# Kernel optimization log

Measured on AMD Instinct MI355X. Metric: run time of the kernel, lower is better.

The kernel has to match this reference:

```python
import jax, jax.numpy as jnp
import numpy as np
import math

B, S, T, D, H = 4, 1024, 1024, 512, 8
EPS = 1e-5

def setup_inputs() -> dict:
    key = jax.random.key(0)
    ks = iter(jax.random.split(key, 40))
    w = lambda *shp: jax.random.normal(next(ks), shp, jnp.float32) * 0.02
    inp = {
        'x': jax.random.normal(next(ks), (B, S, D), jnp.float32),
        'encod_out': jax.random.normal(next(ks), (B, T, D), jnp.float32),
    }
    for p in ('sa', 'ca'):
        inp[p + '_wq'] = w(H, D, D); inp[p + '_bq'] = w(H, D)
        inp[p + '_wk'] = w(H, D, D); inp[p + '_bk'] = w(H, D)
        inp[p + '_wv'] = w(H, D, D); inp[p + '_bv'] = w(H, D)
        inp[p + '_wo'] = w(H, D, D); inp[p + '_bo'] = w(H, D)
        inp[p + '_wf'] = w(H * D, D); inp[p + '_bf'] = w(D)
    for i in (1, 2, 3):
        inp[f'ln{i}_g'] = jnp.ones((D,), jnp.float32)
        inp[f'ln{i}_b'] = jnp.zeros((D,), jnp.float32)
    inp['fc1_w'] = w(D, 4 * D); inp['fc1_b'] = w(4 * D)
    inp['fc2_w'] = w(4 * D, D); inp['fc2_b'] = w(D)
    return inp

def _ln(x, g, b):
    m = jnp.mean(x, -1, keepdims=True)
    v = jnp.mean((x - m) ** 2, -1, keepdims=True)
    return (x - m) / jnp.sqrt(v + EPS) * g + b

def _mha(xq, xkv, wq, bq, wk, bk, wv, bv, wo, bo, wf, bf, mask):
    # per-head FULL-width projections, stacked on head axis h
    Q = jnp.einsum('bsd,hdf->bhsf', xq, wq) + bq[None, :, None, :]
    K = jnp.einsum('btd,hdf->bhtf', xkv, wk) + bk[None, :, None, :]
    V = jnp.einsum('btd,hdf->bhtf', xkv, wv) + bv[None, :, None, :]
    scores = jnp.einsum('bhsf,bhtf->bhst', Q, K) / math.sqrt(Q.shape[-1])
    if mask is not None:
        scores = jnp.where(mask == 0, -jnp.inf, scores)
    A = jax.nn.softmax(scores, axis=-1)
    O = jnp.einsum('bhst,bhtf->bhsf', A, V)
    O = jnp.einsum('bhsf,hfg->bhsg', O, wo) + bo[None, :, None, :]  # per-head out_linear
    cat = O.transpose(0, 2, 1, 3).reshape(O.shape[0], O.shape[2], -1)  # [B,S,H*D]
    return cat @ wf + bf

def reference(x, encod_out,
              sa_wq, sa_bq, sa_wk, sa_bk, sa_wv, sa_bv, sa_wo, sa_bo, sa_wf, sa_bf,
              ca_wq, ca_bq, ca_wk, ca_bk, ca_wv, ca_bv, ca_wo, ca_bo, ca_wf, ca_bf,
              ln1_g, ln1_b, ln2_g, ln2_b, ln3_g, ln3_b,
              fc1_w, fc1_b, fc2_w, fc2_b):
    s = x.shape[1]
    mask = jnp.tril(jnp.ones((s, s), x.dtype))
    h = _mha(x, x, sa_wq, sa_bq, sa_wk, sa_bk, sa_wv, sa_bv, sa_wo, sa_bo, sa_wf, sa_bf, mask)
    x1 = _ln(h + x, ln1_g, ln1_b)
    h = _mha(x1, encod_out, ca_wq, ca_bq, ca_wk, ca_bk, ca_wv, ca_bv, ca_wo, ca_bo, ca_wf, ca_bf, None)
    x2 = _ln(h + x1, ln2_g, ln2_b)
    ff = jax.nn.relu(x2 @ fc1_w + fc1_b) @ fc2_w + fc2_b
    return _ln(ff + x2, ln3_g, ln3_b)
```

## Files before the change

### kernel.cpp

```cpp
#include <hip/hip_runtime.h>
#include <hip/hip_bf16.h>

typedef __hip_bfloat16 bf16;
typedef __attribute__((ext_vector_type(8))) __bf16 bf16x8;
typedef __attribute__((ext_vector_type(4))) float f32x4;

typedef const __attribute__((address_space(1))) void cg_void;
typedef __attribute__((address_space(3))) void lds_void;

__device__ inline float b2f(bf16 v) { return __bfloat162float(v); }
__device__ inline bf16 f2b(float v) { return __float2bfloat16(v); }
__device__ inline float ldf(const float* p) { return *p; }
__device__ inline float ldf(const bf16* p) { return __bfloat162float(*p); }

#define BKK 32

template<int N> __device__ __forceinline__ void wait_vm() {
  if constexpr (N == 0) asm volatile("s_waitcnt vmcnt(0)" ::: "memory");
  else if constexpr (N == 3) asm volatile("s_waitcnt vmcnt(3)" ::: "memory");
  else if constexpr (N == 6) asm volatile("s_waitcnt vmcnt(6)" ::: "memory");
  else asm volatile("s_waitcnt vmcnt(4)" ::: "memory");
}

template<int BM_, int BN_, bool BIAS, bool RELU, bool OUT_BF16>
__global__ __launch_bounds__(256, 2) void gemm_bt(
    const bf16* __restrict__ A, const bf16* __restrict__ Bt, void* __restrict__ Cout,
    const float* __restrict__ bias,
    int M, int N, int K, int lda, int ldb, int ldc,
    long aHi, long aLo, long bHi, long bLo, long cHi, long cLo, int zdiv, int cmode)
{
  constexpr int MI = BM_ / 32;
  constexpr int NJ = BN_ / 32;
  constexpr int NLA = BM_ / 64;
  constexpr int NLB = BN_ / 64;
  constexpr int NL = NLA + NLB;
  alignas(16) __shared__ bf16 As[3][BM_ * BKK];
  alignas(16) __shared__ bf16 Bs[3][BN_ * BKK];
  const int t = threadIdx.x;
  const int l = t & 63;
  const int w = t >> 6;

  const int gx = gridDim.x;
  const long gxy = (long)gx * gridDim.y;
  long flat = (long)blockIdx.z * gxy + (long)blockIdx.y * gx + blockIdx.x;
  const long total = gxy * gridDim.z;
  if ((total & 7) == 0) flat = (flat & 7) * (total >> 3) + (flat >> 3);
  const int z = (int)(flat / gxy);
  const int rem = (int)(flat % gxy);
  const int m0 = (rem % gx) * BM_;
  const int n0 = (rem / gx) * BN_;

  if (cmode == 1 && n0 >= m0 + BM_) return;

  const int zq = z / zdiv, zr = z % zdiv;
  A += (long)zq * aHi + (long)zr * aLo;
  Bt += (long)zq * bHi + (long)zr * bLo;
  const long cbase = (long)zq * cHi + (long)zr * cLo;

  f32x4 acc[MI][NJ] = {};

  const int r0 = t >> 2;
  const int kcs = ((t & 3) ^ ((t >> 3) & 3)) * 8;
  const bf16* aP0 = A + (long)(m0 + r0) * lda + kcs;
  const bf16* bP0 = Bt + (long)(n0 + r0) * ldb + kcs;

  const int fr = l & 15;
  const int qa = (fr >> 1) & 3;
  const int fko = ((l >> 4) ^ qa) << 3;
  const int aRow = (w >> 1) * (BM_ / 2) + fr;
  const int bRow = (w & 1) * (BN_ / 2) + fr;

  const int kLim = (cmode == 2) ? (m0 + BM_ < K ? m0 + BM_ : K) : K;
  const int nt = kLim >> 5;

  auto stage = [&](int tt, int bi) {
    const long kt = (long)tt * BKK;
#pragma unroll
    for (int u = 0; u < NLA; ++u)
      __builtin_amdgcn_global_load_lds((cg_void*)(aP0 + (long)u * 64 * lda + kt),
                                       (lds_void*)(&As[bi][(t + u * 256) * 8]), 16, 0, 0);
#pragma unroll
    for (int u = 0; u < NLB; ++u)
      __builtin_amdgcn_global_load_lds((cg_void*)(bP0 + (long)u * 64 * ldb + kt),
                                       (lds_void*)(&Bs[bi][(t + u * 256) * 8]), 16, 0, 0);
  };

  stage(0, 0);
  stage(1, 1);
  wait_vm<NL>();
  __builtin_amdgcn_s_barrier();

  int bi = 0;
  for (int tt = 0; tt < nt; ++tt) {
    if (tt + 2 < nt) stage(tt + 2, bi == 0 ? 2 : bi - 1);
    bf16x8 af[MI], bv[NJ];
#pragma unroll
    for (int i = 0; i < MI; ++i)
      af[i] = *(const bf16x8*)(&As[bi][(aRow + i * 16) * BKK + fko]);
#pragma unroll
    for (int j = 0; j < NJ; ++j)
      bv[j] = *(const bf16x8*)(&Bs[bi][(bRow + j * 16) * BKK + fko]);
#pragma unroll
    for (int i = 0; i < MI; ++i)
#pragma unroll
      for (int j = 0; j < NJ; ++j)
        acc[i][j] = __builtin_amdgcn_mfma_f32_16x16x32_bf16(af[i], bv[j], acc[i][j], 0, 0, 0);
    if (tt + 1 < nt) {
      if (tt + 2 < nt) wait_vm<NL>();
      else wait_vm<0>();
      __builtin_amdgcn_s_barrier();
    }
    bi = (bi == 2) ? 0 : bi + 1;
  }

  float* cf = (float*)Cout;
  bf16* cb = (bf16*)Cout;
#pragma unroll
  for (int i = 0; i < MI; ++i) {
    const int mb = m0 + (w >> 1) * (BM_ / 2) + i * 16 + ((l >> 4) << 2);
#pragma unroll
    for (int j = 0; j < NJ; ++j) {
      const int nc = n0 + (w & 1) * (BN_ / 2) + j * 16 + fr;
      const float bvv = BIAS ? bias[nc] : 0.f;
#pragma unroll
      for (int r = 0; r < 4; ++r) {
        const int m = mb + r;
        const long off = cbase + (long)m * ldc + nc;
        float vv = acc[i][j][r] + bvv;
        if (RELU) vv = fmaxf(vv, 0.f);
        if (OUT_BF16) cb[off] = f2b(vv);
        else cf[off] = vv;
      }
    }
  }
}

template<int BM_, int BN_, bool B_, bool R_, bool O_>
static inline void gemmL(hipStream_t st, int M, int N, int K,
                         const bf16* A, int lda, long aHi, long aLo,
                         const bf16* Bt, int ldb, long bHi, long bLo,
                         void* C, int ldc, long cHi, long cLo,
                         int zdiv, int nz, const float* bias, int cmode = 0)
{
  dim3 g(M / BM_, N / BN_, nz);
  gemm_bt<BM_, BN_, B_, R_, O_><<<g, dim3(256), 0, st>>>(
      A, Bt, C, bias, M, N, K, lda, ldb, ldc, aHi, aLo, bHi, bLo, cHi, cLo, zdiv, cmode);
}

template<typename ST>
__global__ __launch_bounds__(256) void transpose_to_bf16(
    const ST* __restrict__ in, bf16* __restrict__ out, int R, int C, long sIn, long sOut)
{
  __shared__ bf16 tile[32][33];
  const int z = blockIdx.z;
  in += (long)z * sIn;
  out += (long)z * sOut;
  const int tx = threadIdx.x & 31, ty = threadIdx.x >> 5;
  const int c0 = blockIdx.x * 32, r0 = blockIdx.y * 32;
#pragma unroll
  for (int i = 0; i < 4; ++i)
    tile[ty + i * 8][tx] = f2b(ldf(in + (long)(r0 + ty + i * 8) * C + c0 + tx));
  __syncthreads();
#pragma unroll
  for (int i = 0; i < 4; ++i)
    out[(long)(c0 + ty + i * 8) * R + r0 + tx] = tile[tx][ty + i * 8];
}

__global__ __launch_bounds__(256) void cast4_k(
    const float* __restrict__ in, bf16* __restrict__ out, long n4)
{
  long i = (long)blockIdx.x * 256 + threadIdx.x;
  const long st = (long)gridDim.x * 256;
  for (; i < n4; i += st) {
    const float4 v = ((const float4*)in)[i];
    bf16* o = out + i * 4;
    o[0] = f2b(v.x); o[1] = f2b(v.y); o[2] = f2b(v.z); o[3] = f2b(v.w);
  }
}

__global__ __launch_bounds__(256) void cast4x4_k(
    const float* __restrict__ p0, const float* __restrict__ p1,
    const float* __restrict__ p2, const float* __restrict__ p3,
    bf16* __restrict__ o0, bf16* __restrict__ o1,
    bf16* __restrict__ o2, bf16* __restrict__ o3, long n4)
{
  const float* in; bf16* out;
  switch (blockIdx.y) {
    case 0: in = p0; out = o0; break;
    case 1: in = p1; out = o1; break;
    case 2: in = p2; out = o2; break;
    default: in = p3; out = o3; break;
  }
  long i = (long)blockIdx.x * 256 + threadIdx.x;
  const long st = (long)gridDim.x * 256;
  for (; i < n4; i += st) {
    const float4 v = ((const float4*)in)[i];
    bf16* o = out + i * 4;
    o[0] = f2b(v.x); o[1] = f2b(v.y); o[2] = f2b(v.z); o[3] = f2b(v.w);
  }
}

__global__ __launch_bounds__(256) void fill_sentinel(float* __restrict__ out, long n)
{
  long i = (long)blockIdx.x * 256 + threadIdx.x;
  const long st = (long)gridDim.x * 256;
  for (; i < n; i += st) out[i] = 1.0e6f;
}

__global__ __launch_bounds__(256) void softmax_rows(
    bf16* __restrict__ S, const float* __restrict__ v, float scale, int causal)
{
  const int r = blockIdx.x * 4 + (threadIdx.x >> 6);
  const int l = threadIdx.x & 63;
  const int zl = r >> 10, s = r & 1023;
  bf16* row = S + (long)r * 1024;
  const float* vp = v + (zl >> 2) * 4096 + (zl & 3) * 1024;
  const int t0 = l * 16;
  bf16x8* rp = (bf16x8*)(row + t0);
  const bf16x8 a0 = rp[0], a1 = rp[1];
  float xx[16];
#pragma unroll
  for (int j = 0; j < 8; ++j) { xx[j] = (float)a0[j]; xx[8 + j] = (float)a1[j]; }
  float mx = -3.4e38f;
#pragma unroll
  for (int k = 0; k < 16; ++k) {
    const int tt = t0 + k;
    float val = (xx[k] + vp[tt]) * scale;
    if (causal && tt > s) val = -3.4e38f;
    xx[k] = val;
    mx = fmaxf(mx, val);
  }
#pragma unroll
  for (int d = 1; d < 64; d <<= 1) mx = fmaxf(mx, __shfl_xor(mx, d));
  float sum = 0.f;
#pragma unroll
  for (int k = 0; k < 16; ++k) {
    const float e = (xx[k] > -1e37f) ? __expf(xx[k] - mx) : 0.f;
    xx[k] = e;
    sum += e;
  }
#pragma unroll
  for (int d = 1; d < 64; d <<= 1) sum += __shfl_xor(sum, d);
  const float inv = 1.f / sum;
  bf16x8 r0v, r1v;
#pragma unroll
  for (int j = 0; j < 8; ++j) {
    r0v[j] = (__bf16)(xx[j] * inv);
    r1v[j] = (__bf16)(xx[8 + j] * inv);
  }
  rp[0] = r0v;
  rp[1] = r1v;
}

__global__ __launch_bounds__(256) void ln_fused(
    const float* __restrict__ parts, long zstride, int nz,
    const float* __restrict__ beff, const float* __restrict__ resF,
    const bf16* __restrict__ resB, const float* __restrict__ g,
    const float* __restrict__ b, bf16* __restrict__ outB, float* __restrict__ outF)
{
  const int m = blockIdx.x * 4 + (threadIdx.x >> 6);
  const int l = threadIdx.x & 63;
  float vv[8];
  float s = 0.f;
#pragma unroll
  for (int i = 0; i < 8; ++i) {
    const int c = i * 64 + l;
    float acc = beff[c];
    if (resF) acc += resF[(long)m * 512 + c];
    else acc += b2f(resB[(long)m * 512 + c]);
    for (int zz = 0; zz < nz; ++zz) acc += parts[zz * zstride + (long)m * 512 + c];
    vv[i] = acc;
    s += acc;
  }
#pragma unroll
  for (int d = 1; d < 64; d <<= 1) s += __shfl_xor(s, d);
  const float mean = s * (1.f / 512.f);
  float vs = 0.f;
#pragma unroll
  for (int i = 0; i < 8; ++i) { const float dv = vv[i] - mean; vs += dv * dv; }
#pragma unroll
  for (int d = 1; d < 64; d <<= 1) vs += __shfl_xor(vs, d);
  const float rstd = rsqrtf(vs * (1.f / 512.f) + 1e-5f);
#pragma unroll
  for (int i = 0; i < 8; ++i) {
    const int c = i * 64 + l;
    const float y = (vv[i] - mean) * rstd * g[c] + b[c];
    if (outB) outB[(long)m * 512 + c] = f2b(y);
    if (outF) outF[(long)m * 512 + c] = y;
  }
}

__global__ void beff_init_k(const float* __restrict__ bf_, float* __restrict__ beff)
{
  const int e = blockIdx.x * 256 + threadIdx.x;
  if (e < 512) beff[e] = bf_[e];
}

__global__ __launch_bounds__(256) void beff_wf_k(
    const float* __restrict__ bo, const float* __restrict__ wf, float* __restrict__ beff)
{
  const int t = threadIdx.x;
  const int r0 = blockIdx.x * 128;
  float s0 = 0.f, s1 = 0.f;
  for (int r = 0; r < 128; ++r) {
    const float bb = bo[r0 + r];
    const float* row = wf + (long)(r0 + r) * 512;
    s0 += bb * row[t];
    s1 += bb * row[t + 256];
  }
  atomicAdd(&beff[t], s0);
  atomicAdd(&beff[t + 256], s1);
}

__global__ __launch_bounds__(256) void beff_w2_k(
    const float* __restrict__ bv, const bf16* __restrict__ W2t, float* __restrict__ beff)
{
  const int e = blockIdx.x * 4 + (threadIdx.x >> 6);
  const int l = threadIdx.x & 63;
  const bf16* row = W2t + (long)e * 4096;
  float s = 0.f;
#pragma unroll
  for (int j = 0; j < 8; ++j) {
    const int hf = j * 512 + l * 8;
    const bf16x8 wv = *(const bf16x8*)(row + hf);
    const float4 b0 = *(const float4*)(bv + hf);
    const float4 b1 = *(const float4*)(bv + hf + 4);
    s += (float)wv[0] * b0.x + (float)wv[1] * b0.y + (float)wv[2] * b0.z + (float)wv[3] * b0.w;
    s += (float)wv[4] * b1.x + (float)wv[5] * b1.y + (float)wv[6] * b1.z + (float)wv[7] * b1.w;
  }
#pragma unroll
  for (int d = 1; d < 64; d <<= 1) s += __shfl_xor(s, d);
  if (l == 0) atomicAdd(&beff[e], s);
}

__global__ __launch_bounds__(256) void wkbq_k(
    const float* __restrict__ wk, const float* __restrict__ bq, float* __restrict__ o)
{
  const int id = blockIdx.x * 4 + (threadIdx.x >> 6);
  const int l = threadIdx.x & 63;
  const int h = id >> 9, d = id & 511;
  const float* wp = wk + (long)h * 262144 + (long)d * 512 + l * 8;
  const float* bp = bq + h * 512 + l * 8;
  float s = 0.f;
#pragma unroll
  for (int j = 0; j < 2; ++j) {
    const float4 a = *(const float4*)(wp + j * 4);
    const float4 b = *(const float4*)(bp + j * 4);
    s += a.x * b.x + a.y * b.y + a.z * b.z + a.w * b.w;
  }
#pragma unroll
  for (int dd = 1; dd < 64; dd <<= 1) s += __shfl_xor(s, dd);
  if (l == 0) o[id] = s;
}

__global__ __launch_bounds__(256) void rank1_v(
    const bf16* __restrict__ kvB, const float* __restrict__ wkbq, float* __restrict__ v)
{
  const int m = blockIdx.x * 4 + (threadIdx.x >> 6);
  const int l = threadIdx.x & 63;
  const bf16x8 row = *(const bf16x8*)(kvB + (long)m * 512 + l * 8);
  float rf[8];
#pragma unroll
  for (int j = 0; j < 8; ++j) rf[j] = (float)row[j];
  for (int h = 0; h < 8; ++h) {
    const float* wp = wkbq + h * 512 + l * 8;
    float p = 0.f;
#pragma unroll
    for (int j = 0; j < 8; ++j) p += rf[j] * wp[j];
#pragma unroll
    for (int d = 1; d < 64; d <<= 1) p += __shfl_xor(p, d);
    if (l == 0) v[(long)h * 4096 + m] = p;
  }
}

extern "C" void kernel_launch(void* const* d_in, const int* in_sizes, int n_in,
                              void* d_out, int out_size, void* d_ws, size_t ws_size,
                              hipStream_t stream)
{
  (void)in_sizes; (void)n_in;
  const float* x = (const float*)d_in[0];
  const float* enc = (const float*)d_in[1];
  const float* ln_g[3] = {(const float*)d_in[22], (const float*)d_in[24], (const float*)d_in[26]};
  const float* ln_b[3] = {(const float*)d_in[23], (const float*)d_in[25], (const float*)d_in[27]};
  const float* fc1_w = (const float*)d_in[28];
  const float* fc1_b = (const float*)d_in[29];
  const float* fc2_w = (const float*)d_in[30];
  const float* fc2_b = (const float*)d_in[31];

  const float scale = 0.044194173824159216f;
  char* base = (char*)d_ws;
  const long MB = 1024 * 1024;

  bf16* Xb    = (bf16*)(base + 0 * MB);
  bf16* Eb    = (bf16*)(base + 4 * MB);
  bf16* x1b   = (bf16*)(base + 8 * MB);
  bf16* x2b   = (bf16*)(base + 12 * MB);
  bf16* fc1T  = (bf16*)(base + 16 * MB);
  bf16* fc2T  = (bf16*)(base + 18 * MB);
  float* vbuf = (float*)(base + 20 * MB);
  float* wkbq = (float*)(base + 20 * MB + 256 * 1024);
  float* beff = (float*)(base + 20 * MB + 512 * 1024);
  bf16* XT    = (bf16*)(base + 21 * MB);
  bf16* WqkT  = (bf16*)(base + 25 * MB);
  bf16* W3cat = (bf16*)(base + 29 * MB);
  bf16* T     = (bf16*)(base + 33 * MB);
  float* parts = (float*)(base + 65 * MB);
  bf16* scores = (bf16*)(base + 97 * MB);
  bf16* AX    = (bf16*)(base + 161 * MB);
  bf16* wqB   = (bf16*)(base + 97 * MB);
  bf16* wkB   = (bf16*)(base + 101 * MB);
  bf16* wvB   = (bf16*)(base + 105 * MB);
  bf16* woB   = (bf16*)(base + 109 * MB);
  bf16* wfT   = (bf16*)(base + 113 * MB);
  bf16* W2t   = (bf16*)(base + 117 * MB);
  bf16* Hb    = (bf16*)(base + 97 * MB);

  if (ws_size < (size_t)(193 * MB)) {
    fill_sentinel<<<dim3(2048), dim3(256), 0, stream>>>((float*)d_out, (long)out_size);
    return;
  }

  cast4_k<<<dim3(512), dim3(256), 0, stream>>>(x, Xb, 4096L * 512 / 4);
  cast4_k<<<dim3(512), dim3(256), 0, stream>>>(enc, Eb, 4096L * 512 / 4);
  transpose_to_bf16<float><<<dim3(64, 16, 1), dim3(256), 0, stream>>>(fc1_w, fc1T, 512, 2048, 0, 0);
  transpose_to_bf16<float><<<dim3(16, 64, 1), dim3(256), 0, stream>>>(fc2_w, fc2T, 2048, 512, 0, 0);

  auto run_attn = [&](int ib, const bf16* qB, const bf16* kvB,
                      const float* resF, const bf16* resB, int causal,
                      const float* lg, const float* lb, bf16* outB) {
    const float* wq = (const float*)d_in[ib + 0];
    const float* bq = (const float*)d_in[ib + 1];
    const float* wk = (const float*)d_in[ib + 2];
    const float* wv = (const float*)d_in[ib + 4];
    const float* bv = (const float*)d_in[ib + 5];
    const float* wo = (const float*)d_in[ib + 6];
    const float* bo = (const float*)d_in[ib + 7];
    const float* wf = (const float*)d_in[ib + 8];
    const float* bfv = (const float*)d_in[ib + 9];

    cast4x4_k<<<dim3(512, 4), dim3(256), 0, stream>>>(
        wq, wk, wv, wo, wqB, wkB, wvB, woB, 2097152 / 4);
    transpose_to_bf16<float><<<dim3(16, 128, 1), dim3(256), 0, stream>>>(wf, wfT, 4096, 512, 0, 0);
    gemmL<128, 64, false, false, true>(stream, 512, 512, 512,
        wfT, 4096, 512, 0, woB, 512, 262144, 0, W2t, 4096, 512, 0, 1, 8, nullptr);
    beff_init_k<<<dim3(2), dim3(256), 0, stream>>>(bfv, beff);
    beff_wf_k<<<dim3(32), dim3(256), 0, stream>>>(bo, wf, beff);
    beff_w2_k<<<dim3(128), dim3(256), 0, stream>>>(bv, W2t, beff);
    gemmL<128, 64, false, false, true>(stream, 512, 512, 512,
        wkB, 512, 262144, 0, wqB, 512, 262144, 0, WqkT, 512, 262144, 0, 1, 8, nullptr);
    gemmL<128, 64, false, false, true>(stream, 512, 512, 512,
        W2t, 4096, 512, 0, wvB, 512, 262144, 0, W3cat, 4096, 512, 0, 1, 8, nullptr);
    wkbq_k<<<dim3(1024), dim3(256), 0, stream>>>(wk, bq, wkbq);
    rank1_v<<<dim3(1024), dim3(256), 0, stream>>>(kvB, wkbq, vbuf);
    transpose_to_bf16<bf16><<<dim3(16, 32, 4), dim3(256), 0, stream>>>(
        kvB, XT, 1024, 512, 524288, 524288);
    gemmL<256, 128, false, false, true>(stream, 4096, 4096, 512,
        qB, 512, 0, 0, WqkT, 512, 0, 0, T, 4096, 0, 0, 1, 1, nullptr);

    gemmL<256, 128, false, false, true>(stream, 1024, 1024, 512,
        T, 4096, 512, 4194304,
        kvB, 512, 0, 524288,
        scores, 1024, 4194304, 1048576, 4, 32, nullptr, causal ? 1 : 0);
    softmax_rows<<<dim3(8192), dim3(256), 0, stream>>>(scores, vbuf, scale, causal);
    gemmL<256, 128, false, false, true>(stream, 1024, 512, 1024,
        scores, 1024, 4194304, 1048576,
        XT, 1024, 0, 524288,
        AX, 4096, 512, 4194304, 4, 32, nullptr, causal ? 2 : 0);
    gemmL<256, 128, false, false, false>(stream, 4096, 512, 1024,
        AX, 4096, 1024, 0, W3cat, 4096, 1024, 0,
        parts, 512, 2097152, 0, 1, 4, nullptr);
    ln_fused<<<dim3(1024), dim3(256), 0, stream>>>(
        parts, 2097152, 4, beff, resF, resB, lg, lb, outB, nullptr);
  };

  run_attn(2, Xb, Xb, x, nullptr, 1, ln_g[0], ln_b[0], x1b);
  run_attn(12, x1b, Eb, nullptr, x1b, 0, ln_g[1], ln_b[1], x2b);

  gemmL<256, 128, true, true, true>(stream, 4096, 2048, 512,
      x2b, 512, 0, 0, fc1T, 512, 0, 0, Hb, 2048, 0, 0, 1, 1, fc1_b);
  gemmL<256, 128, false, false, false>(stream, 4096, 512, 512,
      Hb, 2048, 512, 0, fc2T, 2048, 512, 0, parts, 512, 2097152, 0, 1, 4, nullptr);
  ln_fused<<<dim3(1024), dim3(256), 0, stream>>>(
      parts, 2097152, 4, fc2_b, nullptr, x2b, ln_g[2], ln_b[2], nullptr, (float*)d_out);
}
```

Before: 786.7 us.

## Add 256x256 eight-wave MFMA GEMM with interleaved prefetch for attention and FFN

Adds a new 512-thread GEMM kernel with 256x256 tiles, a 64-wide K step and double-buffered direct-to-LDS loads. Prefetch of the next tile is split into quarters interleaved with MFMA phases, with s_setprio raised around the compute blocks. The projection, score, AV and output GEMMs use it, and the split-K GEMMs now use 8 partial slices instead of 4 to keep enough blocks in flight for the larger tiles. This raises workspace size and partial-sum traffic for the LayerNorm reduce, and large tiles can cut occupancy and waste work at the causal edges.

```diff
diff --git a/kernel.cpp b/kernel.cpp
--- a/kernel.cpp
+++ b/kernel.cpp
@@ -20,6 +20,183 @@
   else if constexpr (N == 3) asm volatile("s_waitcnt vmcnt(3)" ::: "memory");
   else if constexpr (N == 6) asm volatile("s_waitcnt vmcnt(6)" ::: "memory");
   else asm volatile("s_waitcnt vmcnt(4)" ::: "memory");
+}
+
+template<bool OUT_BF16>
+__global__ __launch_bounds__(512, 2) void gemm8(
+    const bf16* __restrict__ A, const bf16* __restrict__ Bt, void* __restrict__ Cout,
+    int M, int N, int K, int lda, int ldb, int ldc,
+    long aHi, long aLo, long bHi, long bLo, long cHi, long cLo, int zdiv, int cmode)
+{
+  alignas(16) __shared__ bf16 As[2][256 * 64];
+  alignas(16) __shared__ bf16 Bs[2][256 * 64];
+  const int t = threadIdx.x;
+  const int l = t & 63;
+  const int wid = t >> 6;
+  const int wr = wid >> 2;
+  const int wc = wid & 3;
+
+  const int gx = gridDim.x;
+  const long gxy = (long)gx * gridDim.y;
+  long flat = (long)blockIdx.z * gxy + (long)blockIdx.y * gx + blockIdx.x;
+  const long total = gxy * gridDim.z;
+  if ((total & 7) == 0) flat = (flat & 7) * (total >> 3) + (flat >> 3);
+  const int z = (int)(flat / gxy);
+  const int rem = (int)(flat % gxy);
+  const int m0 = (rem % gx) * 256;
+  const int n0 = (rem / gx) * 256;
+  if (cmode == 1 && n0 >= m0 + 256) return;
+
+  const int zq = z / zdiv, zr = z % zdiv;
+  A += (long)zq * aHi + (long)zr * aLo;
+  Bt += (long)zq * bHi + (long)zr * bLo;
+  const long cbase = (long)zq * cHi + (long)zr * cLo;
+
+  const int srow = l >> 3;
+  const int skc8 = ((l & 7) ^ srow) * 8;
+  const bf16* aS[2];
+  const bf16* bS[2];
+  aS[0] = A + (long)(m0 + wid * 16 + srow) * lda + skc8;
+  aS[1] = A + (long)(m0 + wid * 16 + 8 + srow) * lda + skc8;
+  bS[0] = Bt + (long)(n0 + wid * 16 + srow) * ldb + skc8;
+  bS[1] = Bt + (long)(n0 + wid * 16 + 8 + srow) * ldb + skc8;
+
+  auto stageA = [&](int tt, int bsel, int half) {
+    const long kt = (long)tt * 64;
+#pragma unroll
+    for (int u = 0; u < 2; ++u)
+      __builtin_amdgcn_global_load_lds(
+          (cg_void*)(aS[u] + (long)half * 128 * lda + kt),
+          (lds_void*)(&As[bsel][half * 8192 + wid * 1024 + u * 512]), 16, 0, 0);
+  };
+  auto stageB = [&](int tt, int bsel, int half) {
+    const long kt = (long)tt * 64;
+#pragma unroll
+    for (int u = 0; u < 2; ++u)
+      __builtin_amdgcn_global_load_lds(
+          (cg_void*)(bS[u] + (long)half * 128 * ldb + kt),
+          (lds_void*)(&Bs[bsel][half * 8192 + wid * 1024 + u * 512]), 16, 0, 0);
+  };
+
+  const int fr = l & 15;
+  const int ck0 = (((l >> 4)) ^ (fr & 7)) * 8;
+  const int aBase = (wr * 128 + fr) * 64;
+  const int bBase = (wc * 64 + fr) * 64;
+
+  const int kLim = (cmode == 2) ? (m0 + 256 < K ? m0 + 256 : K) : K;
+  const int nt = kLim >> 6;
+
+  f32x4 acc[8][4] = {};
+  bf16x8 a0[4], a1[4], b0[4], b1[4];
+
+  stageA(0, 0, 0); stageA(0, 0, 1); stageB(0, 0, 0); stageB(0, 0, 1);
+  asm volatile("s_waitcnt vmcnt(0)" ::: "memory");
+  __builtin_amdgcn_s_barrier();
+
+  for (int tt = 0; tt < nt; ++tt) {
+    const int b = tt & 1;
+    const bool pf = (tt + 1 < nt);
+    const bf16* Ab = &As[b][0];
+    const bf16* Bb = &Bs[b][0];
+
+#pragma unroll
+    for (int j = 0; j < 4; ++j) {
+      b0[j] = *(const bf16x8*)(Bb + bBase + j * 1024 + ck0);
+      b1[j] = *(const bf16x8*)(Bb + bBase + j * 1024 + (ck0 ^ 32));
+    }
+#pragma unroll
+    for (int i = 0; i < 4; ++i) {
+      a0[i] = *(const bf16x8*)(Ab + aBase + i * 1024 + ck0);
+      a1[i] = *(const bf16x8*)(Ab + aBase + i * 1024 + (ck0 ^ 32));
+    }
+    if (pf) stageA(tt + 1, b ^ 1, 0);
+    __builtin_amdgcn_s_barrier();
+    __builtin_amdgcn_s_setprio(1);
+#pragma unroll
+    for (int i = 0; i < 4; ++i)
+#pragma unroll
+      for (int j = 0; j < 2; ++j) {
+        acc[i][j] = __builtin_amdgcn_mfma_f32_16x16x32_bf16(a0[i], b0[j], acc[i][j], 0, 0, 0);
+        acc[i][j] = __builtin_amdgcn_mfma_f32_16x16x32_bf16(a1[i], b1[j], acc[i][j], 0, 0, 0);
+      }
+    __builtin_amdgcn_s_setprio(0);
+    __builtin_amdgcn_s_barrier();
+
+    if (pf) stageA(tt + 1, b ^ 1, 1);
+    __builtin_amdgcn_s_barrier();
+    __builtin_amdgcn_s_setprio(1);
+#pragma unroll
+    for (int i = 0; i < 4; ++i)
+#pragma unroll
+      for (int j = 2; j < 4; ++j) {
+        acc[i][j] = __builtin_amdgcn_mfma_f32_16x16x32_bf16(a0[i], b0[j], acc[i][j], 0, 0, 0);
+        acc[i][j] = __builtin_amdgcn_mfma_f32_16x16x32_bf16(a1[i], b1[j], acc[i][j], 0, 0, 0);
+      }
+    __builtin_amdgcn_s_setprio(0);
+    __builtin_amdgcn_s_barrier();
+
+#pragma unroll
+    for (int i = 0; i < 4; ++i) {
+      a0[i] = *(const bf16x8*)(Ab + aBase + 4096 + i * 1024 + ck0);
+      a1[i] = *(const bf16x8*)(Ab + aBase + 4096 + i * 1024 + (ck0 ^ 32));
+    }
+    if (pf) stageB(tt + 1, b ^ 1, 0);
+    __builtin_amdgcn_s_barrier();
+    __builtin_amdgcn_s_setprio(1);
+#pragma unroll
+    for (int i = 0; i < 4; ++i)
+#pragma unroll
+      for (int j = 0; j < 2; ++j) {
+        acc[4 + i][j] = __builtin_amdgcn_mfma_f32_16x16x32_bf16(a0[i], b0[j], acc[4 + i][j], 0, 0, 0);
+        acc[4 + i][j] = __builtin_amdgcn_mfma_f32_16x16x32_bf16(a1[i], b1[j], acc[4 + i][j], 0, 0, 0);
+      }
+    __builtin_amdgcn_s_setprio(0);
+    __builtin_amdgcn_s_barrier();
+
+    if (pf) stageB(tt + 1, b ^ 1, 1);
+    __builtin_amdgcn_s_barrier();
+    __builtin_amdgcn_s_setprio(1);
+#pragma unroll
+    for (int i = 0; i < 4; ++i)
+#pragma unroll
+      for (int j = 2; j < 4; ++j) {
+        acc[4 + i][j] = __builtin_amdgcn_mfma_f32_16x16x32_bf16(a0[i], b0[j], acc[4 + i][j], 0, 0, 0);
+        acc[4 + i][j] = __builtin_amdgcn_mfma_f32_16x16x32_bf16(a1[i], b1[j], acc[4 + i][j], 0, 0, 0);
+      }
+    __builtin_amdgcn_s_setprio(0);
+    if (pf) asm volatile("s_waitcnt vmcnt(0)" ::: "memory");
+    __builtin_amdgcn_s_barrier();
+  }
+
+  float* cf = (float*)Cout;
+  bf16* cb = (bf16*)Cout;
+#pragma unroll
+  for (int i = 0; i < 8; ++i) {
+    const int mb = m0 + wr * 128 + i * 16 + ((l >> 4) << 2);
+#pragma unroll
+    for (int j = 0; j < 4; ++j) {
+      const int nc = n0 + wc * 64 + j * 16 + fr;
+#pragma unroll
+      for (int r = 0; r < 4; ++r) {
+        const long off = cbase + (long)(mb + r) * ldc + nc;
+        const float vv = acc[i][j][r];
+        if (OUT_BF16) cb[off] = f2b(vv);
+        else cf[off] = vv;
+      }
+    }
+  }
+}
+
+template<bool O_>
+static inline void gemm8L(hipStream_t st, int M, int N, int K,
+                          const bf16* A, int lda, long aHi, long aLo,
+                          const bf16* Bt, int ldb, long bHi, long bLo,
+                          void* C, int ldc, long cHi, long cLo,
+                          int zdiv, int nz, int cmode = 0)
+{
+  dim3 g(M / 256, N / 256, nz);
+  gemm8<O_><<<g, dim3(512), 0, st>>>(
+      A, Bt, C, M, N, K, lda, ldb, ldc, aHi, aLo, bHi, bLo, cHi, cLo, zdiv, cmode);
 }
 
 template<int BM_, int BN_, bool BIAS, bool RELU, bool OUT_BF16>
@@ -404,18 +581,18 @@
   bf16* WqkT  = (bf16*)(base + 25 * MB);
   bf16* W3cat = (bf16*)(base + 29 * MB);
   bf16* T     = (bf16*)(base + 33 * MB);
-  float* parts = (float*)(base + 65 * MB);
-  bf16* scores = (bf16*)(base + 97 * MB);
-  bf16* AX    = (bf16*)(base + 161 * MB);
-  bf16* wqB   = (bf16*)(base + 97 * MB);
-  bf16* wkB   = (bf16*)(base + 101 * MB);
-  bf16* wvB   = (bf16*)(base + 105 * MB);
-  bf16* woB   = (bf16*)(base + 109 * MB);
-  bf16* wfT   = (bf16*)(base + 113 * MB);
-  bf16* W2t   = (bf16*)(base + 117 * MB);
-  bf16* Hb    = (bf16*)(base + 97 * MB);
-
-  if (ws_size < (size_t)(193 * MB)) {
+  bf16* scores = (bf16*)(base + 65 * MB);
+  bf16* AX    = (bf16*)(base + 129 * MB);
+  float* parts = (float*)(base + 161 * MB);
+  bf16* wqB   = (bf16*)(base + 65 * MB);
+  bf16* wkB   = (bf16*)(base + 69 * MB);
+  bf16* wvB   = (bf16*)(base + 73 * MB);
+  bf16* woB   = (bf16*)(base + 77 * MB);
+  bf16* wfT   = (bf16*)(base + 81 * MB);
+  bf16* W2t   = (bf16*)(base + 85 * MB);
+  bf16* Hb    = (bf16*)(base + 65 * MB);
+
+  if (ws_size < (size_t)(225 * MB)) {
     fill_sentinel<<<dim3(2048), dim3(256), 0, stream>>>((float*)d_out, (long)out_size);
     return;
   }
@@ -454,23 +631,21 @@
     rank1_v<<<dim3(1024), dim3(256), 0, stream>>>(kvB, wkbq, vbuf);
     transpose_to_bf16<bf16><<<dim3(16, 32, 4), dim3(256), 0, stream>>>(
         kvB, XT, 1024, 512, 524288, 524288);
-    gemmL<256, 128, false, false, true>(stream, 4096, 4096, 512,
-        qB, 512, 0, 0, WqkT, 512, 0, 0, T, 4096, 0, 0, 1, 1, nullptr);
-
-    gemmL<256, 128, false, false, true>(stream, 1024, 1024, 512,
-        T, 4096, 512, 4194304,
-        kvB, 512, 0, 524288,
-        scores, 1024, 4194304, 1048576, 4, 32, nullptr, causal ? 1 : 0);
+
+    gemm8L<true>(stream, 4096, 4096, 512,
+        qB, 512, 0, 0, WqkT, 512, 0, 0, T, 4096, 0, 0, 1, 1, 0);
+    gemm8L<true>(stream, 1024, 1024, 512,
+        T, 4096, 512, 4194304, kvB, 512, 0, 524288,
+        scores, 1024, 4194304, 1048576, 4, 32, causal ? 1 : 0);
     softmax_rows<<<dim3(8192), dim3(256), 0, stream>>>(scores, vbuf, scale, causal);
-    gemmL<256, 128, false, false, true>(stream, 1024, 512, 1024,
-        scores, 1024, 4194304, 1048576,
-        XT, 1024, 0, 524288,
-        AX, 4096, 512, 4194304, 4, 32, nullptr, causal ? 2 : 0);
-    gemmL<256, 128, false, false, false>(stream, 4096, 512, 1024,
-        AX, 4096, 1024, 0, W3cat, 4096, 1024, 0,
-        parts, 512, 2097152, 0, 1, 4, nullptr);
+    gemm8L<true>(stream, 1024, 512, 1024,
+        scores, 1024, 4194304, 1048576, XT, 1024, 0, 524288,
+        AX, 4096, 512, 4194304, 4, 32, causal ? 2 : 0);
+    gemm8L<false>(stream, 4096, 512, 512,
+        AX, 4096, 512, 0, W3cat, 4096, 512, 0,
+        parts, 512, 2097152, 0, 1, 8, 0);
     ln_fused<<<dim3(1024), dim3(256), 0, stream>>>(
-        parts, 2097152, 4, beff, resF, resB, lg, lb, outB, nullptr);
+        parts, 2097152, 8, beff, resF, resB, lg, lb, outB, nullptr);
   };
 
   run_attn(2, Xb, Xb, x, nullptr, 1, ln_g[0], ln_b[0], x1b);
@@ -478,8 +653,8 @@
 
   gemmL<256, 128, true, true, true>(stream, 4096, 2048, 512,
       x2b, 512, 0, 0, fc1T, 512, 0, 0, Hb, 2048, 0, 0, 1, 1, fc1_b);
-  gemmL<256, 128, false, false, false>(stream, 4096, 512, 512,
-      Hb, 2048, 512, 0, fc2T, 2048, 512, 0, parts, 512, 2097152, 0, 1, 4, nullptr);
+  gemm8L<false>(stream, 4096, 512, 256,
+      Hb, 2048, 256, 0, fc2T, 2048, 256, 0, parts, 512, 2097152, 0, 1, 8, 0);
   ln_fused<<<dim3(1024), dim3(256), 0, stream>>>(
-      parts, 2097152, 4, fc2_b, nullptr, x2b, ln_g[2], ln_b[2], nullptr, (float*)d_out);
-}
+      parts, 2097152, 8, fc2_b, nullptr, x2b, ln_g[2], ln_b[2], nullptr, (float*)d_out);
+}
```

New measurement: 789.0 us. About the same (+0.3%).
